# Performance work log

Hardware: AMD Instinct MI355X
Metric: run time of the kernel (lower is better)

## Reference

```python
import jax, jax.numpy as jnp
from jax import lax
import numpy as np

N, M, S = 16, 32, 128
ALPHA = 1e-06


def _conv(x, w, b, stride):
    y = lax.conv_general_dilated(x, w, (stride, stride), [(1, 1), (1, 1)],
                                 dimension_numbers=('NCHW', 'OIHW', 'NCHW'))
    return y + b[None, :, None, None]


def _deconv(x, w, b):
    # torch ConvTranspose2d(k=4, s=2, p=1); torch weight layout [in, out, kh, kw]
    k = jnp.transpose(w, (1, 0, 2, 3))[:, :, ::-1, ::-1]
    y = lax.conv_general_dilated(x, k, (1, 1), [(2, 2), (2, 2)],
                                 lhs_dilation=(2, 2),
                                 dimension_numbers=('NCHW', 'OIHW', 'NCHW'))
    return y + b[None, :, None, None]


def _kaiming(key, shape):
    fan_in = shape[1] * shape[2] * shape[3]
    return jax.random.normal(key, shape, dtype=jnp.float32) * np.float32(np.sqrt(2.0 / fan_in))


def setup_inputs():
    key = jax.random.key(0)
    ks = jax.random.split(key, 12)
    B, H, W = 8, 256, 256
    return {
        'x': jax.random.normal(ks[0], (B, 3, H, W), dtype=jnp.float32),
        'e0n_w1': _kaiming(ks[1], (N, 3, 3, 3)), 'e0n_b1': jnp.zeros((N,), jnp.float32),
        'e0n_w2': _kaiming(ks[2], (N, N, 3, 3)), 'e0n_b2': jnp.zeros((N,), jnp.float32),
        'e0s_w1': _kaiming(ks[3], (S, 3, 3, 3)), 'e0s_b1': jnp.zeros((S,), jnp.float32),
        'e0s_w2': _kaiming(ks[4], (S, S, 3, 3)), 'e0s_b2': jnp.zeros((S,), jnp.float32),
        'd0_dw': jax.random.normal(ks[5], (S, 3, 4, 4), jnp.float32) * np.float32(np.sqrt(2.0 / (3 * 16))),
        'd0_db': jnp.zeros((3,), jnp.float32),
        'd0_cw': _kaiming(ks[6], (3, 3, 3, 3)), 'd0_cb': jnp.zeros((3,), jnp.float32),
        'cell_k': jax.random.normal(ks[7], (M, N), jnp.float32) / np.float32(np.sqrt(N)),
        'cell_v': jax.random.normal(ks[8], (M, S), jnp.float32) / np.float32(np.sqrt(S)),
    }


def reference(x, e0n_w1, e0n_b1, e0n_w2, e0n_b2, e0s_w1, e0s_b1, e0s_w2, e0s_b2,
              d0_dw, d0_db, d0_cw, d0_cb, cell_k, cell_v):
    silu = jax.nn.silu
    # ConvBlock encoders (stride-2 on second conv)
    e0_n = silu(_conv(silu(_conv(x, e0n_w1, e0n_b1, 1)), e0n_w2, e0n_b2, 2))  # [B,N,H/2,W/2]
    e0_s = silu(_conv(silu(_conv(x, e0s_w1, e0s_b1, 1)), e0s_w2, e0s_b2, 2))  # [B,S,H/2,W/2]
    B, _, H, W = e0_n.shape
    # permute+flatten to token streams (the irregular-access glue)
    z = e0_n.transpose(0, 2, 3, 1).reshape(-1, N)        # [T, N]
    t_star = e0_s.transpose(0, 2, 3, 1).reshape(-1, S)   # [T, S]
    # memcell: softmax key/value retrieval over M slots
    w = jax.nn.softmax(z @ cell_k.T / jnp.sqrt(jnp.float32(N)), axis=-1)  # [T, M]
    t_hat = w @ cell_v                                   # read_update's read (old memory)
    cell_v_new = cell_v + ALPHA * (w.T @ (t_star - t_hat))  # delta-rule value update
    t_read = w @ cell_v_new                              # read(); d1_n == e0_n so weights reused
    d0_m = t_read.reshape(B, H, W, S).transpose(0, 3, 1, 2)  # [B,S,H/2,W/2]
    # DeconvBlock decoder back to 3 channels at full resolution
    d0_n = silu(_conv(silu(_deconv(d0_m, d0_dw, d0_db)), d0_cw, d0_cb, 1))
    return d0_n
```

## Files before the change

kernel.cpp:

```cpp
#include <hip/hip_runtime.h>
#include <hip/hip_bf16.h>


#define ALPHA_F 1e-6f
#define TTOT 131072

typedef __attribute__((ext_vector_type(8))) short bf16x8;
typedef __attribute__((ext_vector_type(4))) float f32x4;

__device__ __forceinline__ float silu_f(float x) {
    return x * __builtin_amdgcn_rcpf(1.f + __expf(-x));
}

__device__ __forceinline__ short f2bf(float f) {
    __hip_bfloat16 h = __float2bfloat16(f);
    union { __hip_bfloat16 b; short s; } u; u.b = h; return u.s;
}

__device__ __forceinline__ float bf2f(unsigned short s) {
    union { unsigned u; float f; } c; c.u = (unsigned)s << 16; return c.f;
}

__device__ __forceinline__ int pack_fp8x4(float a, float b, float c, float d) {
    int lo = __builtin_amdgcn_cvt_pk_fp8_f32(a, b, 0, false);
    return  __builtin_amdgcn_cvt_pk_fp8_f32(c, d, lo, true);
}

template<int CO>
__global__ __launch_bounds__(256) void conv1_silu(
    const float* __restrict__ x, const float* __restrict__ wgt,
    const float* __restrict__ bias, float* __restrict__ out)
{
    int idx = blockIdx.x * 256 + threadIdx.x;
    int w = idx & 255, h = (idx >> 8) & 255, b = idx >> 16;
    const float* xb = x + (size_t)b * 3 * 65536;
    float in[27];
#pragma unroll
    for (int ci = 0; ci < 3; ci++)
#pragma unroll
        for (int ky = 0; ky < 3; ky++)
#pragma unroll
            for (int kx = 0; kx < 3; kx++) {
                int hh = h + ky - 1, ww = w + kx - 1;
                bool ok = ((unsigned)hh < 256u) && ((unsigned)ww < 256u);
                in[(ci * 3 + ky) * 3 + kx] = ok ? xb[(ci << 16) + (hh << 8) + ww] : 0.f;
            }
    float* ob = out + (size_t)b * CO * 65536 + (h << 8) + w;
#pragma unroll 4
    for (int co = 0; co < CO; co++) {
        float acc = bias[co];
#pragma unroll
        for (int k = 0; k < 27; k++) acc += in[k] * wgt[co * 27 + k];
        ob[(size_t)co << 16] = silu_f(acc);
    }
}

#define XPAD_DW 842112
__global__ __launch_bounds__(256) void sprep_kern(
    const float* __restrict__ x, const float* __restrict__ w1,
    unsigned* __restrict__ xpad, unsigned* __restrict__ wbf)
{
    if (blockIdx.x == 3290) {
        int co = threadIdx.x;
        if (co < 128) {
            unsigned short row[28];
#pragma unroll
            for (int k = 0; k < 27; k++) row[k] = (unsigned short)f2bf(w1[co * 27 + k]);
            row[27] = 0;
#pragma unroll
            for (int j = 0; j < 14; j++)
                wbf[co * 20 + j] = (unsigned)row[2 * j] | ((unsigned)row[2 * j + 1] << 16);
#pragma unroll
            for (int j = 14; j < 20; j++) wbf[co * 20 + j] = 0u;
        }
        return;
    }
    int d = blockIdx.x * 256 + threadIdx.x;
    if (d >= XPAD_DW) return;
    int w2 = d % 136;
    int rr = d / 136;
    int hp = rr % 258;
    int plane = rr / 258;
    unsigned val = 0u;
    if (hp >= 1 && hp <= 256 && w2 >= 4 && w2 <= 131) {
        const float* src = x + (size_t)plane * 65536 + (size_t)(hp - 1) * 256 + (2 * w2 - 8);
        float2 f = *(const float2*)src;
        val = (unsigned)(unsigned short)f2bf(f.x) |
              ((unsigned)(unsigned short)f2bf(f.y) << 16);
    }
    xpad[d] = val;
}

#define C1K 40
__global__ __launch_bounds__(256) void conv1s_mfma(
    const unsigned short* __restrict__ xpad, const unsigned short* __restrict__ wbf,
    const float* __restrict__ bias, char* __restrict__ out8)
{
    __shared__ __align__(16) short Ps[128 * C1K];
    int tid = threadIdx.x;
    int g = blockIdx.x;
    int b = g >> 10, rem = g & 1023;
    int hh2 = rem >> 1;
    int h = hh2 >> 1, w0 = (hh2 & 1) * 128;
    int coB = (rem & 1) * 64;

    int lane = tid & 63, wave = tid >> 6;
    int coL = (wave & 1) * 32, pxH = (wave >> 1) * 64;
    int r16 = lane & 15, q = lane >> 4, koff = q * 8;

    bf16x8 af[2];
#pragma unroll
    for (int mt = 0; mt < 2; mt++)
        af[mt] = *(const bf16x8*)&wbf[(coB + coL + mt * 16 + r16) * C1K + koff];

    if (tid < 128) {
        int wpix = w0 + tid;
        const unsigned short* p0 = xpad + ((size_t)(b * 3) * 258 + h) * 272 + 7 + wpix;
        unsigned v[27];
#pragma unroll
        for (int ci = 0; ci < 3; ci++) {
            const unsigned short* pc = p0 + ci * 70176;
#pragma unroll
            for (int ky = 0; ky < 3; ky++)
#pragma unroll
                for (int kx = 0; kx < 3; kx++)
                    v[ci * 9 + ky * 3 + kx] = pc[ky * 272 + kx];
        }
        unsigned dw[16];
#pragma unroll
        for (int i = 0; i < 13; i++) dw[i] = v[2 * i] | (v[2 * i + 1] << 16);
        dw[13] = v[26];
        dw[14] = 0u; dw[15] = 0u;
#pragma unroll
        for (int j = 0; j < 4; j++)
            *(float4*)&Ps[tid * C1K + j * 8] = *(float4*)&dw[j * 4];
    }
    __syncthreads();

    bf16x8 bfr[4];
#pragma unroll
    for (int nt = 0; nt < 4; nt++)
        bfr[nt] = *(bf16x8*)&Ps[(pxH + nt * 16 + r16) * C1K + koff];
    f32x4 acc[2][4];
#pragma unroll
    for (int mt = 0; mt < 2; mt++)
#pragma unroll
        for (int nt = 0; nt < 4; nt++) {
#pragma unroll
            for (int r = 0; r < 4; r++) acc[mt][nt][r] = 0.f;
            acc[mt][nt] = __builtin_amdgcn_mfma_f32_16x16x32_bf16(
                af[mt], bfr[nt], acc[mt][nt], 0, 0, 0);
        }

    int hwb = (h << 8) + w0 + pxH;
    int* ob4 = (int*)out8 + (size_t)b * 8 * 65536 * 4;
#pragma unroll
    for (int mt = 0; mt < 2; mt++) {
        int cb = coB + coL + mt * 16 + q * 4;
        float4 bv = *(const float4*)&bias[cb];
        int cg = (coB + coL + mt * 16) >> 4;
#pragma unroll
        for (int nt = 0; nt < 4; nt++) {
            int hw = hwb + nt * 16 + r16;
            int pk = pack_fp8x4(silu_f(acc[mt][nt][0] + bv.x),
                                silu_f(acc[mt][nt][1] + bv.y),
                                silu_f(acc[mt][nt][2] + bv.z),
                                silu_f(acc[mt][nt][3] + bv.w));
            ob4[((size_t)cg * 65536 + hw) * 4 + q] = pk;
        }
    }
}

__global__ __launch_bounds__(256) void wprep_kern(
    const float* __restrict__ w, int* __restrict__ wt8)
{
    int d = blockIdx.x * 256 + threadIdx.x;
    int pos = d >> 12;
    int rb = (d << 2) & 16383;
    int c16 = rb >> 11, co = (rb >> 4) & 127, e0 = rb & 15;
    float f[4];
#pragma unroll
    for (int j = 0; j < 4; j++) {
        int ci = c16 * 16 + e0 + j;
        f[j] = w[co * 1152 + ci * 9 + pos];
    }
    wt8[d] = pack_fp8x4(f[0], f[1], f[2], f[3]);
}

__global__ __launch_bounds__(256) void conv2s_mfma(
    const char* __restrict__ a8,
    const char* __restrict__ wt8,
    const float* __restrict__ bias, __hip_bfloat16* __restrict__ out)
{
    __shared__ __align__(16) char As[2][4096];
    __shared__ __align__(16) char Bs[2][8192];
    int tid = threadIdx.x;
    int g = blockIdx.x;
    int b = g >> 8, h2 = (g >> 1) & 127, w2base = (g & 1) * 64;
    int lane = tid & 63, wave = tid >> 6;
    int mrow = lane & 15, q = lane >> 4;

    f32x4 acc[2][4];
#pragma unroll
    for (int i = 0; i < 2; i++)
#pragma unroll
        for (int j = 0; j < 4; j++)
#pragma unroll
            for (int r = 0; r < 4; r++) acc[i][j][r] = 0.f;

    const float4* ab4 = (const float4*)a8 + (size_t)b * 8 * 65536;
    const float4* wb4 = (const float4*)wt8;
    int cA = tid >> 6, tokA = tid & 63;
    int sB0 = tid, sB1 = tid + 256;
    int swT = tid & 8;
    int offA = ((q & 1) * 8) ^ (mrow & 8);

    int ps = (h2 == 0) ? 3 : 0;
    int nst = (9 - ps) * 2;

#define C2S_LOAD(s, ra, rb0, rb1) do {                                      \
        int pos_ = ps + ((s) >> 1), cc_ = (s) & 1;                          \
        int ky_ = pos_ / 3, kx_ = pos_ - 3 * ky_;                           \
        int y_ = 2 * h2 - 1 + ky_;                                          \
        int x_ = 2 * (w2base + tokA) - 1 + kx_;                             \
        int pix_ = (y_ << 8) + (x_ & 255);                                  \
        ra = make_float4(0.f, 0.f, 0.f, 0.f);                               \
        if (x_ >= 0) ra = ab4[(size_t)(cc_ * 4 + cA) * 65536 + pix_];       \
        const float4* brow_ = wb4 + pos_ * 1024 + cc_ * 512;                \
        rb0 = brow_[sB0]; rb1 = brow_[sB1];                                 \
    } while (0)

#define C2S_STORE(bufi, ra, rb0, rb1) do {                                  \
        union { float4 v; long l[2]; } uA_, u0_, u1_;                       \
        uA_.v = ra; u0_.v = rb0; u1_.v = rb1;                               \
        *(long*)&As[bufi][tid * 16 + swT]       = uA_.l[0];                 \
        *(long*)&As[bufi][tid * 16 + (8 ^ swT)] = uA_.l[1];                 \
        *(long*)&Bs[bufi][sB0 * 16 + swT]       = u0_.l[0];                 \
        *(long*)&Bs[bufi][sB0 * 16 + (8 ^ swT)] = u0_.l[1];                 \
        *(long*)&Bs[bufi][sB1 * 16 + swT]       = u1_.l[0];                 \
        *(long*)&Bs[bufi][sB1 * 16 + (8 ^ swT)] = u1_.l[1];                 \
    } while (0)

    auto compute = [&](const char* Ab, const char* Bb) {
#pragma unroll
        for (int kc = 0; kc < 2; kc++) {
            int cl = kc * 2 + (q >> 1);
            long afr[4], bfr[2];
#pragma unroll
            for (int mt = 0; mt < 4; mt++)
                afr[mt] = *(const long*)&Ab[(cl * 64 + mt * 16 + mrow) * 16 + offA];
#pragma unroll
            for (int nt = 0; nt < 2; nt++)
                bfr[nt] = *(const long*)&Bb[(cl * 128 + wave * 32 + nt * 16 + mrow) * 16 + offA];
#pragma unroll
            for (int nt = 0; nt < 2; nt++)
#pragma unroll
                for (int mt = 0; mt < 4; mt++)
                    acc[nt][mt] = __builtin_amdgcn_mfma_f32_16x16x32_fp8_fp8(
                        afr[mt], bfr[nt], acc[nt][mt], 0, 0, 0);
        }
    };

    {
        float4 ra, rb0, rb1;
        C2S_LOAD(0, ra, rb0, rb1);
        C2S_STORE(0, ra, rb0, rb1);
    }
    __syncthreads();

    for (int s = 0; s < nst; s += 2) {
        float4 na, nb0, nb1;
        C2S_LOAD(s + 1, na, nb0, nb1);
        compute(As[0], Bs[0]);
        C2S_STORE(1, na, nb0, nb1);
        __syncthreads();
        bool more = (s + 2 < nst);
        if (more) C2S_LOAD(s + 2, na, nb0, nb1);
        compute(As[1], Bs[1]);
        if (more) C2S_STORE(0, na, nb0, nb1);
        __syncthreads();
    }
#undef C2S_LOAD
#undef C2S_STORE

    int rowg = q * 4;
    size_t tbase = (size_t)g * 64;
#pragma unroll
    for (int nt = 0; nt < 2; nt++) {
        int co = wave * 32 + nt * 16 + mrow;
        float bvs = bias[co];
#pragma unroll
        for (int mt = 0; mt < 4; mt++)
#pragma unroll
            for (int r = 0; r < 4; r++) {
                int m = mt * 16 + rowg + r;
                out[(tbase + m) * 128 + co] =
                    __float2bfloat16(silu_f(acc[nt][mt][r] + bvs));
            }
    }
}

__global__ __launch_bounds__(256) void conv2n_fused(
    const float* __restrict__ in, const float* __restrict__ wgt,
    const float* __restrict__ bias, const float* __restrict__ ck,
    float* __restrict__ wout)
{
    int idx = blockIdx.x * 256 + threadIdx.x;
    int w2 = idx & 127, h2 = (idx >> 7) & 127, b = idx >> 14;
    const float* ib = in + (size_t)b * 16 * 65536;
    float acc[16];
#pragma unroll
    for (int co = 0; co < 16; co++) acc[co] = bias[co];
    int h0 = 2 * h2 - 1, w0 = 2 * w2 - 1;
    for (int ci = 0; ci < 16; ci++) {
        float t[9];
#pragma unroll
        for (int ky = 0; ky < 3; ky++)
#pragma unroll
            for (int kx = 0; kx < 3; kx++) {
                int hh = h0 + ky, ww = w0 + kx;
                bool ok = ((unsigned)hh < 256u) && ((unsigned)ww < 256u);
                t[ky * 3 + kx] = ok ? ib[((size_t)ci << 16) + (hh << 8) + ww] : 0.f;
            }
#pragma unroll
        for (int co = 0; co < 16; co++)
#pragma unroll
            for (int k = 0; k < 9; k++)
                acc[co] += t[k] * wgt[(co * 16 + ci) * 9 + k];
    }
    float zv[16];
#pragma unroll
    for (int co = 0; co < 16; co++) zv[co] = silu_f(acc[co]);
    float lg[32]; float mx = -1e30f;
#pragma unroll
    for (int m = 0; m < 32; m++) {
        float a = 0.f;
#pragma unroll
        for (int n = 0; n < 16; n++) a += zv[n] * ck[m * 16 + n];
        a *= 0.25f;
        lg[m] = a; mx = fmaxf(mx, a);
    }
    float s = 0.f;
#pragma unroll
    for (int m = 0; m < 32; m++) { lg[m] = __expf(lg[m] - mx); s += lg[m]; }
    float inv = 1.f / s;
    float4* wp = (float4*)(wout + (size_t)idx * 32);
#pragma unroll
    for (int m = 0; m < 8; m++)
        wp[m] = make_float4(lg[4 * m] * inv, lg[4 * m + 1] * inv,
                            lg[4 * m + 2] * inv, lg[4 * m + 3] * inv);
}

__global__ __launch_bounds__(256) void memcell_acc_kern(
    const float* __restrict__ wmat, const __hip_bfloat16* __restrict__ tstar,
    float* __restrict__ part)
{
    __shared__ float ws[64][32];
    __shared__ float ts[64 * 128];
    int tid = threadIdx.x;
    int sg = tid & 31, mg = tid >> 5;
    int mW = tid & 31, m2 = (tid >> 5) * 4;
    float accT[16], accW[4];
#pragma unroll
    for (int i = 0; i < 16; i++) accT[i] = 0.f;
#pragma unroll
    for (int i = 0; i < 4; i++) accW[i] = 0.f;

#pragma unroll 1
    for (int cc = 0; cc < 2; cc++) {
        int c = blockIdx.x * 2 + cc;
        size_t base = (size_t)c * 64;
        __syncthreads();
        {
            const float4* src = (const float4*)(wmat + base * 32);
            float4* dst = (float4*)&ws[0][0];
#pragma unroll
            for (int i = 0; i < 2; i++) dst[tid + 256 * i] = src[tid + 256 * i];
            const float4* src2 = (const float4*)(tstar + base * 128);
#pragma unroll
            for (int i = 0; i < 4; i++) {
                union { float4 v; unsigned short us[8]; } u;
                u.v = src2[tid + 256 * i];
                float* d = &ts[(tid + 256 * i) * 8];
                float4 lo = make_float4(bf2f(u.us[0]), bf2f(u.us[1]), bf2f(u.us[2]), bf2f(u.us[3]));
                float4 hi = make_float4(bf2f(u.us[4]), bf2f(u.us[5]), bf2f(u.us[6]), bf2f(u.us[7]));
                *(float4*)d = lo; *(float4*)(d + 4) = hi;
            }
        }
        __syncthreads();
        for (int t = 0; t < 64; t++) {
            float4 wv = *(const float4*)&ws[t][mg * 4];
            float4 sv = *(const float4*)&ts[t * 128 + sg * 4];
            accT[0]  += wv.x * sv.x; accT[1]  += wv.x * sv.y; accT[2]  += wv.x * sv.z; accT[3]  += wv.x * sv.w;
            accT[4]  += wv.y * sv.x; accT[5]  += wv.y * sv.y; accT[6]  += wv.y * sv.z; accT[7]  += wv.y * sv.w;
            accT[8]  += wv.z * sv.x; accT[9]  += wv.z * sv.y; accT[10] += wv.z * sv.z; accT[11] += wv.z * sv.w;
            accT[12] += wv.w * sv.x; accT[13] += wv.w * sv.y; accT[14] += wv.w * sv.z; accT[15] += wv.w * sv.w;
            float wa = ws[t][mW];
            float4 wb = *(const float4*)&ws[t][m2];
            accW[0] += wa * wb.x; accW[1] += wa * wb.y;
            accW[2] += wa * wb.z; accW[3] += wa * wb.w;
        }
    }
    float* pb = part + (size_t)blockIdx.x * 5120;
#pragma unroll
    for (int i = 0; i < 16; i++) pb[i * 256 + tid] = accT[i];
#pragma unroll
    for (int i = 0; i < 4; i++) pb[4096 + i * 256 + tid] = accW[i];
}

__global__ __launch_bounds__(256) void memcell_reduce_kern(
    const float* __restrict__ part, float* __restrict__ WtT, float* __restrict__ WtW)
{
    int gid = blockIdx.x * 256 + threadIdx.x;
    int j = gid % 5120, seg = gid / 5120;
    const float* p = part + (size_t)seg * 64 * 5120 + j;
    float s = 0.f;
#pragma unroll 8
    for (int k = 0; k < 64; k++) s += p[(size_t)k * 5120];
    int i = j >> 8, t = j & 255;
    if (j < 4096) {
        int sg = t & 31, mg = t >> 5;
        atomicAdd(&WtT[(mg * 4 + (i >> 2)) * 128 + sg * 4 + (i & 3)], s);
    } else {
        int i2 = i - 16;
        int mW = t & 31, m2 = (t >> 5) * 4;
        atomicAdd(&WtW[mW * 32 + m2 + i2], s);
    }
}

__global__ __launch_bounds__(256) void cvnew_kern(
    const float* __restrict__ cv, const float* __restrict__ WtW,
    const float* __restrict__ WtT, float* __restrict__ cvn)
{
    int idx = blockIdx.x * 256 + threadIdx.x;
    int s = idx & 127, m = idx >> 7;
    float g = WtT[idx];
#pragma unroll
    for (int j = 0; j < 32; j++) g -= WtW[m * 32 + j] * cv[j * 128 + s];
    cvn[idx] = cv[idx] + ALPHA_F * g;
}

__global__ __launch_bounds__(256) void emat_kern(
    const float* __restrict__ cvn, const float* __restrict__ dw, float* __restrict__ E)
{
    int idx = blockIdx.x * 256 + threadIdx.x;
    int m = idx >> 6, j = idx & 63;
    int pos = j >> 2, co = j & 3;
    float s = 0.f;
    if (co < 3) {
        const float* cv = cvn + m * 128;
        for (int ci = 0; ci < 128; ci++)
            s += cv[ci] * dw[ci * 48 + co * 16 + pos];
    }
    E[idx] = s;
}

__global__ __launch_bounds__(256) void tread64_kern(
    const float* __restrict__ wmat, const float* __restrict__ E, float* __restrict__ t64)
{
    int t = blockIdx.x * 256 + threadIdx.x;
    float wv[32];
    const float4* wp = (const float4*)(wmat + (size_t)t * 32);
#pragma unroll
    for (int i = 0; i < 8; i++) {
        float4 v = wp[i];
        wv[4 * i] = v.x; wv[4 * i + 1] = v.y; wv[4 * i + 2] = v.z; wv[4 * i + 3] = v.w;
    }
    f32x4 acc[16];
#pragma unroll
    for (int i = 0; i < 16; i++)
#pragma unroll
        for (int r = 0; r < 4; r++) acc[i][r] = 0.f;
    const f32x4* E4 = (const f32x4*)E;
#pragma unroll 4
    for (int m = 0; m < 32; m++) {
        float wm = wv[m];
#pragma unroll
        for (int i = 0; i < 16; i++) {
            f32x4 e = E4[m * 16 + i];
#pragma unroll
            for (int r = 0; r < 4; r++) acc[i][r] += wm * e[r];
        }
    }
    f32x4* ob = (f32x4*)t64;
#pragma unroll
    for (int i = 0; i < 16; i++)
        ob[(size_t)i * TTOT + t] = acc[i];
}

__global__ __launch_bounds__(256) void dec_gather_kern(
    const float* __restrict__ t64, const float* __restrict__ db, float* __restrict__ out)
{
    int g = blockIdx.x;
    int wb = g & 7, hb = (g >> 3) & 7, b = g >> 6;
    int tx = threadIdx.x & 15, ty = threadIdx.x >> 4;
    int h2 = hb * 16 + ty, w2 = wb * 16 + tx;

    float mh[3], mw[3];
    int ihc[3], iwc[3];
#pragma unroll
    for (int a = 0; a < 3; a++) {
        int v = h2 - 1 + a;
        mh[a] = ((unsigned)v < 128u) ? 1.f : 0.f;
        ihc[a] = v < 0 ? 0 : (v > 127 ? 127 : v);
        v = w2 - 1 + a;
        mw[a] = ((unsigned)v < 128u) ? 1.f : 0.f;
        iwc[a] = v < 0 ? 0 : (v > 127 ? 127 : v);
    }
    float acc[2][2][3];
#pragma unroll
    for (int ph = 0; ph < 2; ph++)
#pragma unroll
        for (int pw = 0; pw < 2; pw++)
#pragma unroll
            for (int co = 0; co < 3; co++) acc[ph][pw][co] = db[co];

    const int RA[4] = {0, 1, 1, 2}, RP[4] = {0, 0, 1, 1}, RK[4] = {3, 1, 2, 0};
    size_t tokb = (size_t)b * 16384;
#pragma unroll
    for (int ri = 0; ri < 4; ri++)
#pragma unroll
        for (int cj = 0; cj < 4; cj++) {
            int a = RA[ri], c = RA[cj];
            float m = mh[a] * mw[c];
            size_t tok = tokb + (ihc[a] << 7) + iwc[c];
            int pos = RK[ri] * 4 + RK[cj];
            float4 v = *(const float4*)&t64[((size_t)pos * TTOT + tok) * 4];
            int ph = RP[ri], pw = RP[cj];
            acc[ph][pw][0] += m * v.x;
            acc[ph][pw][1] += m * v.y;
            acc[ph][pw][2] += m * v.z;
        }
    int h = 2 * h2, w = 2 * w2;
#pragma unroll
    for (int ph = 0; ph < 2; ph++)
#pragma unroll
        for (int co = 0; co < 3; co++) {
            float2 v = make_float2(silu_f(acc[ph][0][co]), silu_f(acc[ph][1][co]));
            *(float2*)&out[(size_t)b * 3 * 65536 + (size_t)co * 65536 + ((size_t)(h + ph) << 8) + w] = v;
        }
}

extern "C" void kernel_launch(void* const* d_in, const int* in_sizes, int n_in,
                              void* d_out, int out_size, void* d_ws, size_t ws_size,
                              hipStream_t stream)
{
    const float* x      = (const float*)d_in[0];
    const float* e0n_w1 = (const float*)d_in[1];
    const float* e0n_b1 = (const float*)d_in[2];
    const float* e0n_w2 = (const float*)d_in[3];
    const float* e0n_b2 = (const float*)d_in[4];
    const float* e0s_w1 = (const float*)d_in[5];
    const float* e0s_b1 = (const float*)d_in[6];
    const float* e0s_w2 = (const float*)d_in[7];
    const float* e0s_b2 = (const float*)d_in[8];
    const float* d0_dw  = (const float*)d_in[9];
    const float* d0_db  = (const float*)d_in[10];
    const float* d0_cw  = (const float*)d_in[11];
    const float* d0_cb  = (const float*)d_in[12];
    const float* cell_k = (const float*)d_in[13];
    const float* cell_v = (const float*)d_in[14];
    float* outp = (float*)d_out;

    char* ws = (char*)d_ws;
    char* a_s8             = ws;
    __hip_bfloat16* t_star = (__hip_bfloat16*)(ws + 134217728);
    float* a_n    = (float*)(ws + 201326592);
    char* wt8     = (char*)(ws + 201326592);
    float* part   = (float*)(ws + 201850880);
    float* Emat   = (float*)(ws + 224000000);
    float* wmat   = (float*)(ws + 243269632);
    float* WtW    = (float*)(ws + 260046848);
    float* WtT    = (float*)(ws + 260050944);
    float* cvn    = (float*)(ws + 260067328);
    float* t64    = (float*)(ws);
    float* dec1   = (float*)(ws + 67108864);
    unsigned* xpad = (unsigned*)(ws + 73400320);
    unsigned* wbf  = (unsigned*)(ws + 76800000);

    sprep_kern<<<3291, 256, 0, stream>>>(x, e0s_w1, xpad, wbf);
    conv1_silu<16><<<2048, 256, 0, stream>>>(x, e0n_w1, e0n_b1, a_n);
    conv2n_fused<<<512, 256, 0, stream>>>(a_n, e0n_w2, e0n_b2, cell_k, wmat);
    wprep_kern<<<144, 256, 0, stream>>>(e0s_w2, (int*)wt8);
    conv1s_mfma<<<8192, 256, 0, stream>>>((const unsigned short*)xpad,
                                          (const unsigned short*)wbf, e0s_b1, a_s8);
    conv2s_mfma<<<2048, 256, 0, stream>>>(a_s8, wt8, e0s_b2, t_star);
    hipMemsetAsync(WtW, 0, (1024 + 4096) * sizeof(float), stream);
    memcell_acc_kern<<<1024, 256, 0, stream>>>(wmat, t_star, part);
    memcell_reduce_kern<<<320, 256, 0, stream>>>(part, WtT, WtW);
    cvnew_kern<<<16, 256, 0, stream>>>(cell_v, WtW, WtT, cvn);
    emat_kern<<<8, 256, 0, stream>>>(cvn, d0_dw, Emat);
    tread64_kern<<<512, 256, 0, stream>>>(wmat, Emat, t64);
    dec_gather_kern<<<512, 256, 0, stream>>>(t64, d0_db, dec1);
    conv1_silu<3><<<2048, 256, 0, stream>>>(dec1, d0_cw, d0_cb, outp);
}
```

Baseline: 281.8 us.

## Store N-branch conv1 output as padded channels-last for vectorized conv2 loads

The 16-channel first conv of the N branch now writes a zero-padded NHWC buffer (258x264 per image), and the stride-2 second conv reads each 3x3 tap as four float4 loads, with no bounds checks. The padding border is zeroed by extra blocks added to the prep kernel, which also transposes the conv2 weights into a [k][ci][co] layout. The goal is to replace strided scalar NCHW gathers with coalesced vector loads. The cost is a slightly larger intermediate buffer and extra prep work.

```diff
diff --git a/kernel.cpp b/kernel.cpp
--- a/kernel.cpp
+++ b/kernel.cpp
@@ -55,14 +55,63 @@
     }
 }
 
+__global__ __launch_bounds__(256) void conv1n_silu(
+    const float* __restrict__ x, const float* __restrict__ wgt,
+    const float* __restrict__ bias, float* __restrict__ anc)
+{
+    int idx = blockIdx.x * 256 + threadIdx.x;
+    int w = idx & 255, h = (idx >> 8) & 255, b = idx >> 16;
+    const float* xb = x + (size_t)b * 3 * 65536;
+    float in[27];
+#pragma unroll
+    for (int ci = 0; ci < 3; ci++)
+#pragma unroll
+        for (int ky = 0; ky < 3; ky++)
+#pragma unroll
+            for (int kx = 0; kx < 3; kx++) {
+                int hh = h + ky - 1, ww = w + kx - 1;
+                bool ok = ((unsigned)hh < 256u) && ((unsigned)ww < 256u);
+                in[(ci * 3 + ky) * 3 + kx] = ok ? xb[(ci << 16) + (hh << 8) + ww] : 0.f;
+            }
+    float o[16];
+#pragma unroll
+    for (int co = 0; co < 16; co++) {
+        float acc = bias[co];
+#pragma unroll
+        for (int k = 0; k < 27; k++) acc += in[k] * wgt[co * 27 + k];
+        o[co] = silu_f(acc);
+    }
+    float* ob = anc + (((size_t)b * 258 + (h + 1)) * 264 + (w + 1)) * 16;
+#pragma unroll
+    for (int j = 0; j < 4; j++) *(float4*)&ob[4 * j] = *(float4*)&o[4 * j];
+}
+
 #define XPAD_DW 842112
 __global__ __launch_bounds__(256) void sprep_kern(
     const float* __restrict__ x, const float* __restrict__ w1,
-    unsigned* __restrict__ xpad, unsigned* __restrict__ wbf)
-{
+    const float* __restrict__ w2n,
+    unsigned* __restrict__ xpad, unsigned* __restrict__ wbf,
+    float* __restrict__ wn, float* __restrict__ anc)
+{
+    if (blockIdx.x >= 3291) {
+        int zidx = (blockIdx.x - 3291) * 256 + threadIdx.x;
+        int b = zidx / 8352, j = zidx % 8352;
+        size_t off;
+        if (j < 4224) {
+            int c = j >> 4, ci = j & 15;
+            off = (((size_t)b * 258 + 0) * 264 + c) * 16 + ci;
+        } else {
+            int j2 = j - 4224;
+            int r = j2 >> 4, ci = j2 & 15;
+            off = (((size_t)b * 258 + r) * 264 + 0) * 16 + ci;
+        }
+        anc[off] = 0.f;
+        return;
+    }
     if (blockIdx.x == 3290) {
-        int co = threadIdx.x;
-        if (co < 128) {
+        int t = threadIdx.x;
+        if (t < 128) {
+            int co = t;
             unsigned short row[28];
 #pragma unroll
             for (int k = 0; k < 27; k++) row[k] = (unsigned short)f2bf(w1[co * 27 + k]);
@@ -72,6 +121,12 @@
                 wbf[co * 20 + j] = (unsigned)row[2 * j] | ((unsigned)row[2 * j + 1] << 16);
 #pragma unroll
             for (int j = 14; j < 20; j++) wbf[co * 20 + j] = 0u;
+        }
+#pragma unroll
+        for (int u = 0; u < 9; u++) {
+            int i = t * 9 + u;
+            int co = i & 15, ci = (i >> 4) & 15, k = i >> 8;
+            wn[i] = w2n[(co * 16 + ci) * 9 + k];
         }
         return;
     }
@@ -301,33 +356,35 @@
 }
 
 __global__ __launch_bounds__(256) void conv2n_fused(
-    const float* __restrict__ in, const float* __restrict__ wgt,
+    const float* __restrict__ anc, const float* __restrict__ wn,
     const float* __restrict__ bias, const float* __restrict__ ck,
     float* __restrict__ wout)
 {
     int idx = blockIdx.x * 256 + threadIdx.x;
     int w2 = idx & 127, h2 = (idx >> 7) & 127, b = idx >> 14;
-    const float* ib = in + (size_t)b * 16 * 65536;
+    const float* pb = anc + (((size_t)b * 258 + 2 * h2) * 264 + 2 * w2) * 16;
     float acc[16];
 #pragma unroll
     for (int co = 0; co < 16; co++) acc[co] = bias[co];
-    int h0 = 2 * h2 - 1, w0 = 2 * w2 - 1;
-    for (int ci = 0; ci < 16; ci++) {
-        float t[9];
-#pragma unroll
-        for (int ky = 0; ky < 3; ky++)
-#pragma unroll
-            for (int kx = 0; kx < 3; kx++) {
-                int hh = h0 + ky, ww = w0 + kx;
-                bool ok = ((unsigned)hh < 256u) && ((unsigned)ww < 256u);
-                t[ky * 3 + kx] = ok ? ib[((size_t)ci << 16) + (hh << 8) + ww] : 0.f;
+#pragma unroll
+    for (int ky = 0; ky < 3; ky++)
+#pragma unroll
+        for (int kx = 0; kx < 3; kx++) {
+            int k = ky * 3 + kx;
+            const float* tp = pb + (ky * 264 + kx) * 16;
+            float tap[16];
+#pragma unroll
+            for (int j = 0; j < 4; j++)
+                *(float4*)&tap[4 * j] = *(const float4*)&tp[4 * j];
+            const float* wk = wn + k * 256;
+#pragma unroll
+            for (int ci = 0; ci < 16; ci++) {
+                float tv = tap[ci];
+#pragma unroll
+                for (int co = 0; co < 16; co++)
+                    acc[co] += tv * wk[ci * 16 + co];
             }
-#pragma unroll
-        for (int co = 0; co < 16; co++)
-#pragma unroll
-            for (int k = 0; k < 9; k++)
-                acc[co] += t[k] * wgt[(co * 16 + ci) * 9 + k];
-    }
+        }
     float zv[16];
 #pragma unroll
     for (int co = 0; co < 16; co++) zv[co] = silu_f(acc[co]);
@@ -565,7 +622,6 @@
     char* ws = (char*)d_ws;
     char* a_s8             = ws;
     __hip_bfloat16* t_star = (__hip_bfloat16*)(ws + 134217728);
-    float* a_n    = (float*)(ws + 201326592);
     char* wt8     = (char*)(ws + 201326592);
     float* part   = (float*)(ws + 201850880);
     float* Emat   = (float*)(ws + 224000000);
@@ -577,10 +633,12 @@
     float* dec1   = (float*)(ws + 67108864);
     unsigned* xpad = (unsigned*)(ws + 73400320);
     unsigned* wbf  = (unsigned*)(ws + 76800000);
-
-    sprep_kern<<<3291, 256, 0, stream>>>(x, e0s_w1, xpad, wbf);
-    conv1_silu<16><<<2048, 256, 0, stream>>>(x, e0n_w1, e0n_b1, a_n);
-    conv2n_fused<<<512, 256, 0, stream>>>(a_n, e0n_w2, e0n_b2, cell_k, wmat);
+    float* wn      = (float*)(ws + 76810240);
+    float* a_nc    = (float*)(ws + 77594624);
+
+    sprep_kern<<<3552, 256, 0, stream>>>(x, e0s_w1, e0n_w2, xpad, wbf, wn, a_nc);
+    conv1n_silu<<<2048, 256, 0, stream>>>(x, e0n_w1, e0n_b1, a_nc);
+    conv2n_fused<<<512, 256, 0, stream>>>(a_nc, wn, e0n_b2, cell_k, wmat);
     wprep_kern<<<144, 256, 0, stream>>>(e0s_w2, (int*)wt8);
     conv1s_mfma<<<8192, 256, 0, stream>>>((const unsigned short*)xpad,
                                           (const unsigned short*)wbf, e0s_b1, a_s8);
```

Result: no change. 284.9 us (+1.1%).
